# Kernel optimization log

Measured on AMD Instinct MI355X. Metric: run time of the kernel, lower is better.

The kernel has to match this reference:

```python
import jax, jax.numpy as jnp
import numpy as np

B, T, DIM = 4, 2048, 1024
H, DH = 16, 64  # num_heads, dim_head; weight_dim = H*DH = 1024
SCALE = DIM ** (-0.5)  # note: original scales by dim**-0.5, not dim_head**-0.5


def setup_inputs() -> dict:
    key = jax.random.key(0)
    k1, k2, k3 = jax.random.split(key, 3)
    x = jax.random.normal(k1, (B, T, DIM), dtype=jnp.float32)
    w_qkv = jax.random.normal(k2, (3 * H * DH, DIM), dtype=jnp.float32) * (DIM ** -0.5)
    w_out = jax.random.normal(k3, (DIM, H * DH), dtype=jnp.float32) * ((H * DH) ** -0.5)
    b_out = jnp.zeros((DIM,), dtype=jnp.float32)
    return {"x": x, "w_qkv": w_qkv, "w_out": w_out, "b_out": b_out}


def reference(x, w_qkv, w_out, b_out):
    # qkv: [b, t, 3*H*DH] (torch Linear: x @ W^T)
    qkv = jnp.einsum('btc,oc->bto', x, w_qkv)
    # rearrange 'b t (d k h) -> k b h t d' with k=3, h=H: d is the OUTERMOST
    # factor of the flattened axis, then k, then h (h fastest-varying).
    qkv = qkv.reshape(B, T, DH, 3, H)          # [b, t, d, k, h]
    qkv = jnp.transpose(qkv, (3, 0, 4, 1, 2))   # [k, b, h, t, d]
    q, k, v = qkv[0], qkv[1], qkv[2]
    # scores: [b, h, t, t]
    attn = jnp.einsum('bhid,bhjd->bhij', q, k) * SCALE
    attn = jax.nn.softmax(attn, axis=-1)
    out = jnp.einsum('bhij,bhjd->bhid', attn, v)           # [b, h, t, d]
    out = jnp.transpose(out, (0, 2, 1, 3)).reshape(B, T, H * DH)  # 'b h t d -> b t (h d)'
    return jnp.einsum('btc,oc->bto', out, w_out) + b_out
```

## Files before the change

kernel.cpp:

```cpp
#include <hip/hip_runtime.h>
#include <hip/hip_bf16.h>


typedef __attribute__((ext_vector_type(8))) short short8;
typedef __attribute__((ext_vector_type(4))) float floatx4;

static __device__ __forceinline__ floatx4 mfma16(short8 a, short8 b, floatx4 c) {
    return __builtin_amdgcn_mfma_f32_16x16x32_bf16(a, b, c, 0, 0, 0);
}

static __device__ __forceinline__ unsigned short f2bf_bits(float f) {
    __hip_bfloat16 h = __float2bfloat16(f);
    return *reinterpret_cast<unsigned short*>(&h);
}

static __device__ __forceinline__ float fast_exp2(float x) {
#if __has_builtin(__builtin_amdgcn_exp2f)
    return __builtin_amdgcn_exp2f(x);
#else
    return exp2f(x);
#endif
}

#define GLD16(gptr, ldsptr)                                                  \
    __builtin_amdgcn_global_load_lds(                                        \
        (const __attribute__((address_space(1))) void*)(gptr),               \
        (__attribute__((address_space(3))) void*)(ldsptr), 16, 0, 0)

__global__ __launch_bounds__(256) void k_cvt(
    const float* __restrict__ src, unsigned short* __restrict__ dst, int n4)
{
    typedef __attribute__((ext_vector_type(4))) unsigned short ushort4v;
    for (int i = blockIdx.x * blockDim.x + threadIdx.x; i < n4;
         i += gridDim.x * blockDim.x) {
        const float4 v = ((const float4*)src)[i];
        ushort4v o;
        o.x = f2bf_bits(v.x);
        o.y = f2bf_bits(v.y);
        o.z = f2bf_bits(v.z);
        o.w = f2bf_bits(v.w);
        ((ushort4v*)dst)[i] = o;
    }
}

__global__ __launch_bounds__(256) void k_qkv(
    const unsigned short* __restrict__ x,
    const unsigned short* __restrict__ wq,
    unsigned short* __restrict__ qb,
    unsigned short* __restrict__ kb,
    unsigned short* __restrict__ vb)
{
    __shared__ unsigned short SM[16384];

    const int tid  = threadIdx.x;
    const int wave = tid >> 6, lane = tid & 63;
    const int quad = lane >> 4, l16 = lane & 15;
    const int wm = wave >> 1, wn = wave & 1;

    const int fid  = blockIdx.y * 24 + blockIdx.x;
    const int nfid = (fid & 7) * 192 + (fid >> 3);
    const int bx = nfid % 24;
    const int m0 = (nfid / 24) * 128;
    const int kk = bx >> 3;
    const int cb = bx & 7;

    const int srow = lane >> 2;
    const int sc8  = (lane & 3) * 8;
    const int row0 = wave * 32 + srow;
    const int row1 = row0 + 16;
    int bn0, bn1;
    if (kk < 2) {
        bn0 = (row0 & 63) * 48 + kk * 16 + cb * 2 + (row0 >> 6);
        bn1 = (row1 & 63) * 48 + kk * 16 + cb * 2 + (row1 >> 6);
    } else {
        bn0 = (cb * 8 + (row0 >> 4)) * 48 + 32 + (row0 & 15);
        bn1 = (cb * 8 + (row1 >> 4)) * 48 + 32 + (row1 & 15);
    }

    floatx4 acc[4][4];
#pragma unroll
    for (int i = 0; i < 4; i++)
#pragma unroll
        for (int j = 0; j < 4; j++) acc[i][j] = (floatx4){0.f, 0.f, 0.f, 0.f};

#define QKV_STAGE(BUF, K0)                                                        \
    do {                                                                          \
        GLD16(&x[(m0 + row0) * 1024 + (K0) + sc8],                                \
              &SM[(BUF) * 8192 + (wave * 32) * 32]);                              \
        GLD16(&x[(m0 + row1) * 1024 + (K0) + sc8],                                \
              &SM[(BUF) * 8192 + (wave * 32 + 16) * 32]);                         \
        GLD16(&wq[bn0 * 1024 + (K0) + sc8],                                       \
              &SM[(BUF) * 8192 + 4096 + (wave * 32) * 32]);                       \
        GLD16(&wq[bn1 * 1024 + (K0) + sc8],                                       \
              &SM[(BUF) * 8192 + 4096 + (wave * 32 + 16) * 32]);                  \
    } while (0)

    QKV_STAGE(0, 0);
    int buf = 0;
    for (int k0 = 0; k0 < 1024; k0 += 32) {
        __syncthreads();
        if (k0 + 32 < 1024) QKV_STAGE(buf ^ 1, k0 + 32);

        const unsigned short* Ab = &SM[buf * 8192];
        const unsigned short* Bb = &SM[buf * 8192 + 4096];
        short8 af[4], bfv[4];
#pragma unroll
        for (int mi = 0; mi < 4; mi++)
            af[mi] = *(const short8*)&Ab[(wm * 64 + mi * 16 + l16) * 32 + quad * 8];
#pragma unroll
        for (int ni = 0; ni < 4; ni++)
            bfv[ni] = *(const short8*)&Bb[(wn * 64 + ni * 16 + l16) * 32 + quad * 8];
#pragma unroll
        for (int mi = 0; mi < 4; mi++)
#pragma unroll
            for (int ni = 0; ni < 4; ni++)
                acc[mi][ni] = mfma16(af[mi], bfv[ni], acc[mi][ni]);
        buf ^= 1;
    }
    __syncthreads();

    if (kk == 2) {
#pragma unroll
        for (int ni = 0; ni < 4; ni++) {
            const int d = cb * 8 + wn * 4 + ni;
#pragma unroll
            for (int mi = 0; mi < 4; mi++) {
                const int m  = m0 + wm * 64 + mi * 16 + quad * 4;
                const int b  = m >> 11;
                const int tt = m & 2047;
                ushort4 pk;
                pk.x = f2bf_bits(acc[mi][ni][0]);
                pk.y = f2bf_bits(acc[mi][ni][1]);
                pk.z = f2bf_bits(acc[mi][ni][2]);
                pk.w = f2bf_bits(acc[mi][ni][3]);
                *(ushort4*)&vb[((b * 16 + l16) * 64 + d) * 2048 + tt] = pk;
            }
        }
    } else {
        const float scale = (kk == 0) ? 0.045084220027780106f : 1.0f;
        unsigned short* dst = (kk == 0) ? qb : kb;
        const int b = m0 >> 11, tt0 = m0 & 2047;
#pragma unroll
        for (int s = 0; s < 2; s++) {
            if (wn == s) {
#pragma unroll
                for (int ni = 0; ni < 4; ni++) {
                    const int d = ni * 16 + l16;
#pragma unroll
                    for (int mi = 0; mi < 4; mi++) {
                        const int tl = wm * 64 + mi * 16 + quad * 4;
#pragma unroll
                        for (int r = 0; r < 4; r++)
                            SM[(tl + r) * 72 + d] = f2bf_bits(acc[mi][ni][r] * scale);
                    }
                }
            }
            __syncthreads();
#pragma unroll
            for (int u = 0; u < 4; u++) {
                const int w  = tid + u * 256;
                const int tl = w >> 3;
                const int ch = (w & 7) * 8;
                *(uint4*)&dst[((b * 16 + cb * 2 + s) * 2048 + tt0 + tl) * 64 + ch] =
                    *(const uint4*)&SM[tl * 72 + ch];
            }
            __syncthreads();
        }
    }
#undef QKV_STAGE
}

__global__ __launch_bounds__(512) void k_attn(
    const unsigned short* __restrict__ qt,
    const unsigned short* __restrict__ kt,
    const unsigned short* __restrict__ vg,
    __hip_bfloat16* __restrict__ og)
{
    __shared__ unsigned short Ks[128 * 72];
    __shared__ unsigned short Vt[64 * 136];
    __shared__ unsigned short Pt[8 * 32 * 72];

    const int tid  = threadIdx.x;
    const int wave = tid >> 6, lane = tid & 63;
    const int quad = lane >> 4, l16 = lane & 15;
    const int blk = blockIdx.x;
    const int bh  = (blk & 7) | ((blk >> 6) << 3);
    const int q0  = ((blk >> 3) & 7) * 256;
    const int qr  = q0 + wave * 32;

    short8 qf[2][2];
#pragma unroll
    for (int mi = 0; mi < 2; mi++)
#pragma unroll
        for (int ks = 0; ks < 2; ks++)
            qf[mi][ks] = *(const short8*)&qt[(bh * 2048 + qr + mi * 16 + l16) * 64 + ks * 32 + quad * 8];

    float lsum[2] = {0.f, 0.f};
    floatx4 o[2][4];
#pragma unroll
    for (int mi = 0; mi < 2; mi++)
#pragma unroll
        for (int di = 0; di < 4; di++) o[mi][di] = (floatx4){0.f, 0.f, 0.f, 0.f};

    const int kr = tid >> 3, kc = (tid & 7) * 8;
    const int vd = tid >> 4, vc = (tid & 15) * 8;

    uint4 rk0 = *(const uint4*)&kt[(bh * 2048 + kr) * 64 + kc];
    uint4 rk1 = *(const uint4*)&kt[(bh * 2048 + 64 + kr) * 64 + kc];
    uint4 rv0 = *(const uint4*)&vg[(bh * 64 + vd) * 2048 + vc];
    uint4 rv1 = *(const uint4*)&vg[(bh * 64 + 32 + vd) * 2048 + vc];

    for (int j0 = 0; j0 < 2048; j0 += 128) {
        *(uint4*)&Ks[kr * 72 + kc]         = rk0;
        *(uint4*)&Ks[(64 + kr) * 72 + kc]  = rk1;
        *(uint4*)&Vt[vd * 136 + vc]        = rv0;
        *(uint4*)&Vt[(32 + vd) * 136 + vc] = rv1;
        __syncthreads();
        if (j0 + 128 < 2048) {
            rk0 = *(const uint4*)&kt[(bh * 2048 + j0 + 128 + kr) * 64 + kc];
            rk1 = *(const uint4*)&kt[(bh * 2048 + j0 + 192 + kr) * 64 + kc];
            rv0 = *(const uint4*)&vg[(bh * 64 + vd) * 2048 + j0 + 128 + vc];
            rv1 = *(const uint4*)&vg[(bh * 64 + 32 + vd) * 2048 + j0 + 128 + vc];
        }

#pragma unroll
        for (int jj = 0; jj < 2; jj++) {
            const int kb0 = jj * 64;

            floatx4 st[2][4];
#pragma unroll
            for (int mi = 0; mi < 2; mi++)
#pragma unroll
                for (int nk = 0; nk < 4; nk++) st[mi][nk] = (floatx4){0.f, 0.f, 0.f, 0.f};
#pragma unroll
            for (int ks = 0; ks < 2; ks++) {
                short8 kf[4];
#pragma unroll
                for (int nk = 0; nk < 4; nk++)
                    kf[nk] = *(const short8*)&Ks[(kb0 + nk * 16 + l16) * 72 + ks * 32 + quad * 8];
                __builtin_amdgcn_s_setprio(1);
#pragma unroll
                for (int mi = 0; mi < 2; mi++)
#pragma unroll
                    for (int nk = 0; nk < 4; nk++)
                        st[mi][nk] = mfma16(kf[nk], qf[mi][ks], st[mi][nk]);
                __builtin_amdgcn_s_setprio(0);
            }

#pragma unroll
            for (int mi = 0; mi < 2; mi++) {
#pragma unroll
                for (int nk = 0; nk < 4; nk++) {
                    const float p0 = fast_exp2(st[mi][nk][0]);
                    const float p1 = fast_exp2(st[mi][nk][1]);
                    const float p2 = fast_exp2(st[mi][nk][2]);
                    const float p3 = fast_exp2(st[mi][nk][3]);
                    lsum[mi] += (p0 + p1) + (p2 + p3);
                    ushort4 pk;
                    pk.x = f2bf_bits(p0);
                    pk.y = f2bf_bits(p1);
                    pk.z = f2bf_bits(p2);
                    pk.w = f2bf_bits(p3);
                    *(ushort4*)&Pt[(wave * 32 + mi * 16 + l16) * 72 + nk * 16 + quad * 4] = pk;
                }
            }
            __builtin_amdgcn_s_waitcnt(0xc07f);

#pragma unroll
            for (int ks = 0; ks < 2; ks++) {
                short8 pf[2], vf[4];
#pragma unroll
                for (int mi = 0; mi < 2; mi++)
                    pf[mi] = *(const short8*)&Pt[(wave * 32 + mi * 16 + l16) * 72 + ks * 32 + quad * 8];
#pragma unroll
                for (int di = 0; di < 4; di++)
                    vf[di] = *(const short8*)&Vt[(di * 16 + l16) * 136 + kb0 + ks * 32 + quad * 8];
                __builtin_amdgcn_s_setprio(1);
#pragma unroll
                for (int mi = 0; mi < 2; mi++)
#pragma unroll
                    for (int di = 0; di < 4; di++)
                        o[mi][di] = mfma16(pf[mi], vf[di], o[mi][di]);
                __builtin_amdgcn_s_setprio(0);
            }
        }
        __syncthreads();
    }

#pragma unroll
    for (int mi = 0; mi < 2; mi++) {
        float t = lsum[mi];
        t += __shfl_xor(t, 16);
        t += __shfl_xor(t, 32);
        lsum[mi] = t;
    }

    const int b = bh >> 4, h = bh & 15;
#pragma unroll
    for (int mi = 0; mi < 2; mi++) {
#pragma unroll
        for (int r = 0; r < 4; r++) {
            const float inv = 1.0f / __shfl(lsum[mi], quad * 4 + r);
            const int t = qr + mi * 16 + quad * 4 + r;
#pragma unroll
            for (int di = 0; di < 4; di++)
                og[(b * 2048 + t) * 1024 + h * 64 + di * 16 + l16] =
                    __float2bfloat16(o[mi][di][r] * inv);
        }
    }
}

__global__ __launch_bounds__(256) void k_out(
    const unsigned short* __restrict__ a,
    const unsigned short* __restrict__ wq,
    const float* __restrict__ bias,
    float* __restrict__ out)
{
    __shared__ unsigned short SM[16384];

    const int tid  = threadIdx.x;
    const int wave = tid >> 6, lane = tid & 63;
    const int quad = lane >> 4, l16 = lane & 15;
    const int wm = wave >> 1, wn = wave & 1;

    const int fid  = blockIdx.y * 8 + blockIdx.x;
    const int nfid = (fid & 7) * 64 + (fid >> 3);
    const int n0 = (nfid & 7) * 128;
    const int m0 = (nfid >> 3) * 128;

    const int srow = lane >> 2;
    const int sc8  = (lane & 3) * 8;
    const int row0 = wave * 32 + srow;
    const int row1 = row0 + 16;

    floatx4 acc[4][4];
#pragma unroll
    for (int i = 0; i < 4; i++)
#pragma unroll
        for (int j = 0; j < 4; j++) acc[i][j] = (floatx4){0.f, 0.f, 0.f, 0.f};

#define OUT_STAGE(BUF, K0)                                                        \
    do {                                                                          \
        GLD16(&a[(m0 + row0) * 1024 + (K0) + sc8],                                \
              &SM[(BUF) * 8192 + (wave * 32) * 32]);                              \
        GLD16(&a[(m0 + row1) * 1024 + (K0) + sc8],                                \
              &SM[(BUF) * 8192 + (wave * 32 + 16) * 32]);                         \
        GLD16(&wq[(n0 + row0) * 1024 + (K0) + sc8],                               \
              &SM[(BUF) * 8192 + 4096 + (wave * 32) * 32]);                       \
        GLD16(&wq[(n0 + row1) * 1024 + (K0) + sc8],                               \
              &SM[(BUF) * 8192 + 4096 + (wave * 32 + 16) * 32]);                  \
    } while (0)

    OUT_STAGE(0, 0);
    int buf = 0;
    for (int k0 = 0; k0 < 1024; k0 += 32) {
        __syncthreads();
        if (k0 + 32 < 1024) OUT_STAGE(buf ^ 1, k0 + 32);

        const unsigned short* Ab = &SM[buf * 8192];
        const unsigned short* Bb = &SM[buf * 8192 + 4096];
        short8 af[4], bfv[4];
#pragma unroll
        for (int mi = 0; mi < 4; mi++)
            af[mi] = *(const short8*)&Ab[(wm * 64 + mi * 16 + l16) * 32 + quad * 8];
#pragma unroll
        for (int ni = 0; ni < 4; ni++)
            bfv[ni] = *(const short8*)&Bb[(wn * 64 + ni * 16 + l16) * 32 + quad * 8];
#pragma unroll
        for (int mi = 0; mi < 4; mi++)
#pragma unroll
            for (int ni = 0; ni < 4; ni++)
                acc[mi][ni] = mfma16(af[mi], bfv[ni], acc[mi][ni]);
        buf ^= 1;
    }
#undef OUT_STAGE

#pragma unroll
    for (int ni = 0; ni < 4; ni++) {
        const int col = n0 + wn * 64 + ni * 16 + l16;
        const float bv = bias[col];
#pragma unroll
        for (int mi = 0; mi < 4; mi++) {
            const int mbase = m0 + wm * 64 + mi * 16 + quad * 4;
#pragma unroll
            for (int r = 0; r < 4; r++)
                out[(mbase + r) * 1024 + col] = acc[mi][ni][r] + bv;
        }
    }
}

extern "C" void kernel_launch(void* const* d_in, const int* in_sizes, int n_in,
                              void* d_out, int out_size, void* d_ws, size_t ws_size,
                              hipStream_t stream) {
    const float* x    = (const float*)d_in[0];
    const float* wqkv = (const float*)d_in[1];
    const float* wout = (const float*)d_in[2];
    const float* bout = (const float*)d_in[3];
    float* out = (float*)d_out;

    unsigned short* ws = (unsigned short*)d_ws;
    unsigned short* xb    = ws;
    unsigned short* wqkvb = xb + 8388608;
    unsigned short* woutb = wqkvb + 3145728;
    unsigned short* qb    = woutb + 1048576;
    unsigned short* kb    = qb + 8388608;
    unsigned short* vb    = kb + 8388608;
    unsigned short* ob    = vb + 8388608;

    k_cvt<<<2048, 256, 0, stream>>>(x,    xb,    8388608 / 4);
    k_cvt<<<1024, 256, 0, stream>>>(wqkv, wqkvb, 3145728 / 4);
    k_cvt<<<512,  256, 0, stream>>>(wout, woutb, 1048576 / 4);

    k_qkv<<<dim3(24, 64), 256, 0, stream>>>(xb, wqkvb, qb, kb, vb);
    k_attn<<<512, 512, 0, stream>>>(qb, kb, vb, (__hip_bfloat16*)ob);
    k_out<<<dim3(8, 64), 256, 0, stream>>>(ob, woutb, bout, out);
}
```

Measured before the change: 268.0 us.

## Rewrite attention with 32x32 MFMA and register-resident P via permlane32 swap

```diff
diff --git a/kernel.cpp b/kernel.cpp
--- a/kernel.cpp
+++ b/kernel.cpp
@@ -4,9 +4,13 @@
 
 typedef __attribute__((ext_vector_type(8))) short short8;
 typedef __attribute__((ext_vector_type(4))) float floatx4;
+typedef __attribute__((ext_vector_type(16))) float floatx16;
 
 static __device__ __forceinline__ floatx4 mfma16(short8 a, short8 b, floatx4 c) {
     return __builtin_amdgcn_mfma_f32_16x16x32_bf16(a, b, c, 0, 0, 0);
+}
+static __device__ __forceinline__ floatx16 mfma32(short8 a, short8 b, floatx16 c) {
+    return __builtin_amdgcn_mfma_f32_32x32x16_bf16(a, b, c, 0, 0, 0);
 }
 
 static __device__ __forceinline__ unsigned short f2bf_bits(float f) {
@@ -19,6 +23,23 @@
     return __builtin_amdgcn_exp2f(x);
 #else
     return exp2f(x);
+#endif
+}
+
+static __device__ __forceinline__ unsigned cvt_pk_bf16(float lo, float hi) {
+    unsigned r;
+    asm("v_cvt_pk_bf16_f32 %0, %1, %2" : "=v"(r) : "v"(lo), "v"(hi));
+    return r;
+}
+
+static __device__ __forceinline__ void plane32_swap(unsigned& x, unsigned& y) {
+#if __has_builtin(__builtin_amdgcn_permlane32_swap)
+    typedef unsigned int uintx2 __attribute__((ext_vector_type(2)));
+    uintx2 r = __builtin_amdgcn_permlane32_swap(x, y, false, false);
+    x = r[0];
+    y = r[1];
+#else
+    asm volatile("v_permlane32_swap_b32 %0, %1" : "+v"(x), "+v"(y));
 #endif
 }
 
@@ -170,142 +191,140 @@
 #undef QKV_STAGE
 }
 
-__global__ __launch_bounds__(512) void k_attn(
+__global__ __launch_bounds__(256, 2) void k_attn(
     const unsigned short* __restrict__ qt,
     const unsigned short* __restrict__ kt,
     const unsigned short* __restrict__ vg,
     __hip_bfloat16* __restrict__ og)
 {
-    __shared__ unsigned short Ks[128 * 72];
-    __shared__ unsigned short Vt[64 * 136];
-    __shared__ unsigned short Pt[8 * 32 * 72];
+    __shared__ unsigned short Ks[64 * 72];
+    __shared__ unsigned short Vt[64 * 72];
 
     const int tid  = threadIdx.x;
     const int wave = tid >> 6, lane = tid & 63;
-    const int quad = lane >> 4, l16 = lane & 15;
+    const int l31  = lane & 31, hi = lane >> 5;
     const int blk = blockIdx.x;
     const int bh  = (blk & 7) | ((blk >> 6) << 3);
     const int q0  = ((blk >> 3) & 7) * 256;
-    const int qr  = q0 + wave * 32;
-
-    short8 qf[2][2];
-#pragma unroll
-    for (int mi = 0; mi < 2; mi++)
-#pragma unroll
-        for (int ks = 0; ks < 2; ks++)
-            qf[mi][ks] = *(const short8*)&qt[(bh * 2048 + qr + mi * 16 + l16) * 64 + ks * 32 + quad * 8];
+    const int qr  = q0 + wave * 64;
+
+    short8 qf[2][4];
+#pragma unroll
+    for (int qb2 = 0; qb2 < 2; qb2++)
+#pragma unroll
+        for (int ks = 0; ks < 4; ks++)
+            qf[qb2][ks] = *(const short8*)
+                &qt[(bh * 2048 + qr + qb2 * 32 + l31) * 64 + ks * 16 + hi * 8];
 
     float lsum[2] = {0.f, 0.f};
-    floatx4 o[2][4];
-#pragma unroll
-    for (int mi = 0; mi < 2; mi++)
-#pragma unroll
-        for (int di = 0; di < 4; di++) o[mi][di] = (floatx4){0.f, 0.f, 0.f, 0.f};
-
-    const int kr = tid >> 3, kc = (tid & 7) * 8;
-    const int vd = tid >> 4, vc = (tid & 15) * 8;
-
-    uint4 rk0 = *(const uint4*)&kt[(bh * 2048 + kr) * 64 + kc];
-    uint4 rk1 = *(const uint4*)&kt[(bh * 2048 + 64 + kr) * 64 + kc];
-    uint4 rv0 = *(const uint4*)&vg[(bh * 64 + vd) * 2048 + vc];
-    uint4 rv1 = *(const uint4*)&vg[(bh * 64 + 32 + vd) * 2048 + vc];
-
-    for (int j0 = 0; j0 < 2048; j0 += 128) {
-        *(uint4*)&Ks[kr * 72 + kc]         = rk0;
-        *(uint4*)&Ks[(64 + kr) * 72 + kc]  = rk1;
-        *(uint4*)&Vt[vd * 136 + vc]        = rv0;
-        *(uint4*)&Vt[(32 + vd) * 136 + vc] = rv1;
+    floatx16 o[2][2];
+#pragma unroll
+    for (int qb2 = 0; qb2 < 2; qb2++)
+#pragma unroll
+        for (int db = 0; db < 2; db++)
+#pragma unroll
+            for (int r = 0; r < 16; r++) o[qb2][db][r] = 0.f;
+
+    const int sr = tid >> 2, sc = (tid & 3) * 16;
+
+    uint4 rka = *(const uint4*)&kt[(bh * 2048 + sr) * 64 + sc];
+    uint4 rkb = *(const uint4*)&kt[(bh * 2048 + sr) * 64 + sc + 8];
+    uint4 rva = *(const uint4*)&vg[(bh * 64 + sr) * 2048 + sc];
+    uint4 rvb = *(const uint4*)&vg[(bh * 64 + sr) * 2048 + sc + 8];
+
+    for (int j0 = 0; j0 < 2048; j0 += 64) {
+        *(uint4*)&Ks[sr * 72 + sc]     = rka;
+        *(uint4*)&Ks[sr * 72 + sc + 8] = rkb;
+        *(uint4*)&Vt[sr * 72 + sc]     = rva;
+        *(uint4*)&Vt[sr * 72 + sc + 8] = rvb;
         __syncthreads();
-        if (j0 + 128 < 2048) {
-            rk0 = *(const uint4*)&kt[(bh * 2048 + j0 + 128 + kr) * 64 + kc];
-            rk1 = *(const uint4*)&kt[(bh * 2048 + j0 + 192 + kr) * 64 + kc];
-            rv0 = *(const uint4*)&vg[(bh * 64 + vd) * 2048 + j0 + 128 + vc];
-            rv1 = *(const uint4*)&vg[(bh * 64 + 32 + vd) * 2048 + j0 + 128 + vc];
-        }
-
-#pragma unroll
-        for (int jj = 0; jj < 2; jj++) {
-            const int kb0 = jj * 64;
-
-            floatx4 st[2][4];
-#pragma unroll
-            for (int mi = 0; mi < 2; mi++)
-#pragma unroll
-                for (int nk = 0; nk < 4; nk++) st[mi][nk] = (floatx4){0.f, 0.f, 0.f, 0.f};
-#pragma unroll
-            for (int ks = 0; ks < 2; ks++) {
-                short8 kf[4];
-#pragma unroll
-                for (int nk = 0; nk < 4; nk++)
-                    kf[nk] = *(const short8*)&Ks[(kb0 + nk * 16 + l16) * 72 + ks * 32 + quad * 8];
-                __builtin_amdgcn_s_setprio(1);
-#pragma unroll
-                for (int mi = 0; mi < 2; mi++)
-#pragma unroll
-                    for (int nk = 0; nk < 4; nk++)
-                        st[mi][nk] = mfma16(kf[nk], qf[mi][ks], st[mi][nk]);
-                __builtin_amdgcn_s_setprio(0);
-            }
-
-#pragma unroll
-            for (int mi = 0; mi < 2; mi++) {
-#pragma unroll
-                for (int nk = 0; nk < 4; nk++) {
-                    const float p0 = fast_exp2(st[mi][nk][0]);
-                    const float p1 = fast_exp2(st[mi][nk][1]);
-                    const float p2 = fast_exp2(st[mi][nk][2]);
-                    const float p3 = fast_exp2(st[mi][nk][3]);
-                    lsum[mi] += (p0 + p1) + (p2 + p3);
-                    ushort4 pk;
-                    pk.x = f2bf_bits(p0);
-                    pk.y = f2bf_bits(p1);
-                    pk.z = f2bf_bits(p2);
-                    pk.w = f2bf_bits(p3);
-                    *(ushort4*)&Pt[(wave * 32 + mi * 16 + l16) * 72 + nk * 16 + quad * 4] = pk;
+        if (j0 + 64 < 2048) {
+            rka = *(const uint4*)&kt[(bh * 2048 + j0 + 64 + sr) * 64 + sc];
+            rkb = *(const uint4*)&kt[(bh * 2048 + j0 + 64 + sr) * 64 + sc + 8];
+            rva = *(const uint4*)&vg[(bh * 64 + sr) * 2048 + j0 + 64 + sc];
+            rvb = *(const uint4*)&vg[(bh * 64 + sr) * 2048 + j0 + 64 + sc + 8];
+        }
+
+#pragma unroll
+        for (int kb2 = 0; kb2 < 2; kb2++) {
+            short8 kf[4];
+#pragma unroll
+            for (int ks = 0; ks < 4; ks++)
+                kf[ks] = *(const short8*)
+                    &Ks[(kb2 * 32 + l31) * 72 + ks * 16 + hi * 8];
+
+            floatx16 st[2];
+#pragma unroll
+            for (int qb2 = 0; qb2 < 2; qb2++)
+#pragma unroll
+                for (int r = 0; r < 16; r++) st[qb2][r] = 0.f;
+            __builtin_amdgcn_s_setprio(1);
+#pragma unroll
+            for (int ks = 0; ks < 4; ks++)
+#pragma unroll
+                for (int qb2 = 0; qb2 < 2; qb2++)
+                    st[qb2] = mfma32(kf[ks], qf[qb2][ks], st[qb2]);
+            __builtin_amdgcn_s_setprio(0);
+
+            short8 paf[2][2];
+#pragma unroll
+            for (int qb2 = 0; qb2 < 2; qb2++) {
+                float p[16];
+#pragma unroll
+                for (int r = 0; r < 16; r++) p[r] = fast_exp2(st[qb2][r]);
+                lsum[qb2] += ((p[0] + p[1]) + (p[2] + p[3])) +
+                             ((p[4] + p[5]) + (p[6] + p[7])) +
+                             ((p[8] + p[9]) + (p[10] + p[11])) +
+                             ((p[12] + p[13]) + (p[14] + p[15]));
+#pragma unroll
+                for (int hf = 0; hf < 2; hf++) {
+                    const int r0 = hf * 8;
+                    unsigned c01 = cvt_pk_bf16(p[r0 + 0], p[r0 + 1]);
+                    unsigned c23 = cvt_pk_bf16(p[r0 + 2], p[r0 + 3]);
+                    unsigned c45 = cvt_pk_bf16(p[r0 + 4], p[r0 + 5]);
+                    unsigned c67 = cvt_pk_bf16(p[r0 + 6], p[r0 + 7]);
+                    plane32_swap(c01, c45);
+                    plane32_swap(c23, c67);
+                    uint4 t4 = {c01, c23, c45, c67};
+                    paf[qb2][hf] = *reinterpret_cast<short8*>(&t4);
                 }
             }
-            __builtin_amdgcn_s_waitcnt(0xc07f);
-
-#pragma unroll
-            for (int ks = 0; ks < 2; ks++) {
-                short8 pf[2], vf[4];
-#pragma unroll
-                for (int mi = 0; mi < 2; mi++)
-                    pf[mi] = *(const short8*)&Pt[(wave * 32 + mi * 16 + l16) * 72 + ks * 32 + quad * 8];
-#pragma unroll
-                for (int di = 0; di < 4; di++)
-                    vf[di] = *(const short8*)&Vt[(di * 16 + l16) * 136 + kb0 + ks * 32 + quad * 8];
-                __builtin_amdgcn_s_setprio(1);
-#pragma unroll
-                for (int mi = 0; mi < 2; mi++)
-#pragma unroll
-                    for (int di = 0; di < 4; di++)
-                        o[mi][di] = mfma16(pf[mi], vf[di], o[mi][di]);
-                __builtin_amdgcn_s_setprio(0);
-            }
+
+            short8 vf[2][2];
+#pragma unroll
+            for (int db = 0; db < 2; db++)
+#pragma unroll
+                for (int hf = 0; hf < 2; hf++)
+                    vf[db][hf] = *(const short8*)
+                        &Vt[(db * 32 + l31) * 72 + kb2 * 32 + hf * 16 + hi * 8];
+            __builtin_amdgcn_s_setprio(1);
+#pragma unroll
+            for (int qb2 = 0; qb2 < 2; qb2++)
+#pragma unroll
+                for (int db = 0; db < 2; db++)
+#pragma unroll
+                    for (int hf = 0; hf < 2; hf++)
+                        o[qb2][db] = mfma32(paf[qb2][hf], vf[db][hf], o[qb2][db]);
+            __builtin_amdgcn_s_setprio(0);
         }
         __syncthreads();
     }
 
-#pragma unroll
-    for (int mi = 0; mi < 2; mi++) {
-        float t = lsum[mi];
-        t += __shfl_xor(t, 16);
-        t += __shfl_xor(t, 32);
-        lsum[mi] = t;
-    }
+    lsum[0] += __shfl_xor(lsum[0], 32);
+    lsum[1] += __shfl_xor(lsum[1], 32);
 
     const int b = bh >> 4, h = bh & 15;
 #pragma unroll
-    for (int mi = 0; mi < 2; mi++) {
-#pragma unroll
-        for (int r = 0; r < 4; r++) {
-            const float inv = 1.0f / __shfl(lsum[mi], quad * 4 + r);
-            const int t = qr + mi * 16 + quad * 4 + r;
-#pragma unroll
-            for (int di = 0; di < 4; di++)
-                og[(b * 2048 + t) * 1024 + h * 64 + di * 16 + l16] =
-                    __float2bfloat16(o[mi][di][r] * inv);
+    for (int qb2 = 0; qb2 < 2; qb2++) {
+#pragma unroll
+        for (int r = 0; r < 16; r++) {
+            const int qrl = (r & 3) + 8 * (r >> 2) + 4 * hi;
+            const float inv = 1.0f / __shfl(lsum[qb2], qrl);
+            const int t = qr + qb2 * 32 + qrl;
+#pragma unroll
+            for (int db = 0; db < 2; db++)
+                og[(b * 2048 + t) * 1024 + h * 64 + db * 32 + l31] =
+                    __float2bfloat16(o[qb2][db][r] * inv);
         }
     }
 }
@@ -412,6 +431,6 @@
     k_cvt<<<512,  256, 0, stream>>>(wout, woutb, 1048576 / 4);
 
     k_qkv<<<dim3(24, 64), 256, 0, stream>>>(xb, wqkvb, qb, kb, vb);
-    k_attn<<<512, 512, 0, stream>>>(qb, kb, vb, (__hip_bfloat16*)ob);
+    k_attn<<<512, 256, 0, stream>>>(qb, kb, vb, (__hip_bfloat16*)ob);
     k_out<<<dim3(8, 64), 256, 0, stream>>>(ob, woutb, bout, out);
 }
```

New measurement: 254.2 us. -5.1%, faster.
